# Performance work log

Measured on AMD Instinct MI355X. Metric: run time of the kernel, lower is better.

The kernel has to match this reference:

```python
import math
import jax, jax.numpy as jnp
import numpy as np

B, S, D = 4, 2048, 1024
NEG = -1e20

def setup_inputs() -> dict:
    key = jax.random.key(0)
    k1, k2, k3, k4 = jax.random.split(key, 4)
    X = jax.random.normal(k1, (B, S, D), dtype=jnp.float32)
    # True = masked position (masked_fill semantics)
    attention_mask = jax.random.randint(k2, (B, S, S), 0, 2).astype(bool)
    scale = 1.0 / math.sqrt(D)
    W_qkv = jax.random.normal(k3, (D, 3 * D), dtype=jnp.float32) * scale
    b_qkv = jnp.zeros((3 * D,), dtype=jnp.float32)
    W_out = jax.random.normal(k4, (D, D), dtype=jnp.float32) * scale
    b_out = jnp.zeros((D,), dtype=jnp.float32)
    return {"X": X, "attention_mask": attention_mask,
            "W_qkv": W_qkv, "b_qkv": b_qkv, "W_out": W_out, "b_out": b_out}

def reference(X, attention_mask, W_qkv, b_qkv, W_out, b_out):
    dim = X.shape[-1]
    QKV = X @ W_qkv + b_qkv                      # [B,S,3D]
    Q, K, V = jnp.split(QKV, 3, axis=-1)         # each [B,S,D]
    scores = jnp.einsum('bqd,bkd->bqk', Q, K) / math.sqrt(dim)  # [B,S,S]
    scores = jnp.where(attention_mask, NEG, scores)
    attn = jax.nn.softmax(scores, axis=-1)       # dropout_rate=0.0 -> identity
    ctx = jnp.einsum('bqk,bkd->bqd', attn, V)    # [B,S,D]
    return ctx @ W_out + b_out
```

## Files before the change

kernel.cpp:

```cpp
#include <hip/hip_runtime.h>
#include <cstdint>
#include <cstddef>

#define BB 4
#define SS 2048
#define DD 1024

typedef _Float16 f16;
typedef _Float16 f16x8 __attribute__((ext_vector_type(8)));
typedef _Float16 f16x4 __attribute__((ext_vector_type(4)));
typedef float fx4 __attribute__((ext_vector_type(4)));

__device__ __forceinline__ void async_copy16(void* lds, const void* g) {
  __builtin_amdgcn_global_load_lds(
      (__attribute__((address_space(1))) void*)const_cast<void*>(g),
      (__attribute__((address_space(3))) void*)lds,
      16, 0, 0);
}

template <typename OutT, bool HAS_BIAS>
__global__ __launch_bounds__(256, 2) void gemm_nt(
    const f16* __restrict__ A, long long strideA, int lda,
    const f16* __restrict__ Bt, long long strideB, int ldb,
    OutT* __restrict__ C, long long strideC, int ldc,
    const float* __restrict__ bias, float scale, int K) {
  __shared__ f16 As[128 * 32];
  __shared__ f16 Bs[128 * 32];

  const int t = threadIdx.x;
  const int lane = t & 63;
  const int wid = t >> 6;
  const long long bz = blockIdx.z;
  const int tileM = blockIdx.y * 128;
  const int tileN = blockIdx.x * 128;

  const f16* Ab = A + bz * strideA;
  const f16* Bb = Bt + bz * strideB;
  OutT* Cb = C + bz * strideC;

  const int sr = t >> 2;
  const int sc = (t & 3) * 8;
  const f16* pa0 = Ab + (size_t)(tileM + sr) * lda + sc;
  const f16* pa1 = Ab + (size_t)(tileM + 64 + sr) * lda + sc;
  const f16* pb0 = Bb + (size_t)(tileN + sr) * ldb + sc;
  const f16* pb1 = Bb + (size_t)(tileN + 64 + sr) * ldb + sc;
  f16* la0 = &As[t * 8];
  f16* la1 = &As[2048 + t * 8];
  f16* lb0 = &Bs[t * 8];
  f16* lb1 = &Bs[2048 + t * 8];

  const int waveM = (wid >> 1) * 64;
  const int waveN = (wid & 1) * 64;
  const int r16 = lane & 15;
  const int quad = lane >> 4;

  fx4 acc[4][4] = {};

  for (int k0 = 0; k0 < K; k0 += 32) {
    async_copy16(la0, pa0 + k0);
    async_copy16(la1, pa1 + k0);
    async_copy16(lb0, pb0 + k0);
    async_copy16(lb1, pb1 + k0);
    __syncthreads();

    f16x8 af[4], bf[4];
#pragma unroll
    for (int i = 0; i < 4; ++i)
      af[i] = *(const f16x8*)&As[(waveM + i * 16 + r16) * 32 + quad * 8];
#pragma unroll
    for (int i = 0; i < 4; ++i)
      bf[i] = *(const f16x8*)&Bs[(waveN + i * 16 + r16) * 32 + quad * 8];

#pragma unroll
    for (int i = 0; i < 4; ++i)
#pragma unroll
      for (int j = 0; j < 4; ++j)
        acc[i][j] =
            __builtin_amdgcn_mfma_f32_16x16x32_f16(af[i], bf[j], acc[i][j], 0, 0, 0);
    __syncthreads();
  }

#pragma unroll
  for (int j = 0; j < 4; ++j) {
    const int col = tileN + waveN + j * 16 + r16;
    const float bv = HAS_BIAS ? bias[col] : 0.0f;
#pragma unroll
    for (int i = 0; i < 4; ++i) {
#pragma unroll
      for (int r = 0; r < 4; ++r) {
        const int row = tileM + waveM + i * 16 + quad * 4 + r;
        Cb[(size_t)row * ldc + col] = (OutT)(acc[i][j][r] * scale + bv);
      }
    }
  }
}

__global__ __launch_bounds__(256) void k_conv(const float* __restrict__ in,
                                              f16* __restrict__ out, int n4) {
  const int i = blockIdx.x * 256 + threadIdx.x;
  if (i >= n4) return;
  const float4 v = ((const float4*)in)[i];
  f16x4 h = {(f16)v.x, (f16)v.y, (f16)v.z, (f16)v.w};
  ((f16x4*)out)[i] = h;
}

__global__ __launch_bounds__(256) void k_transpose_conv(const float* __restrict__ in,
                                                        f16* __restrict__ out, int R,
                                                        int C) {
  __shared__ float tile[32][33];
  const int bx = blockIdx.x * 32;
  const int by = blockIdx.y * 32;
  const int tx = threadIdx.x;
  const int ty = threadIdx.y;
  for (int i = ty; i < 32; i += 8)
    tile[i][tx] = in[(size_t)(by + i) * C + bx + tx];
  __syncthreads();
  for (int i = ty; i < 32; i += 8)
    out[(size_t)(bx + i) * R + by + tx] = (f16)tile[tx][i];
}

__global__ __launch_bounds__(256) void k_transpose_h(const f16* __restrict__ in,
                                                     long long strideIn, int ldin,
                                                     int R, f16* __restrict__ out,
                                                     long long strideOut) {
  const int b = blockIdx.z;
  in += (long long)b * strideIn;
  out += (long long)b * strideOut;
  __shared__ f16 tile[32][33];
  const int bx = blockIdx.x * 32;
  const int by = blockIdx.y * 32;
  const int tx = threadIdx.x;
  const int ty = threadIdx.y;
  for (int i = ty; i < 32; i += 8)
    tile[i][tx] = in[(size_t)(by + i) * ldin + bx + tx];
  __syncthreads();
  for (int i = ty; i < 32; i += 8)
    out[(size_t)(bx + i) * R + by + tx] = tile[tx][i];
}

__global__ __launch_bounds__(256) void k_softmax(const f16* __restrict__ scores,
                                                 const int* __restrict__ mask,
                                                 f16* __restrict__ probs) {
  const int row = blockIdx.x;
  const size_t off = (size_t)row * SS;
  const int t = threadIdx.x;

  const f16x8 sv = *(const f16x8*)(scores + off + t * 8);
  const int4 m0 = ((const int4*)(mask + off + t * 8))[0];
  const int4 m1 = ((const int4*)(mask + off + t * 8))[1];
  const int m[8] = {m0.x, m0.y, m0.z, m0.w, m1.x, m1.y, m1.z, m1.w};

  float v[8];
#pragma unroll
  for (int i = 0; i < 8; ++i) v[i] = m[i] ? -1e20f : (float)sv[i];

  float mx = v[0];
#pragma unroll
  for (int i = 1; i < 8; ++i) mx = fmaxf(mx, v[i]);
#pragma unroll
  for (int d = 32; d; d >>= 1) mx = fmaxf(mx, __shfl_xor(mx, d, 64));

  __shared__ float redm[4];
  __shared__ float reds[4];
  if ((t & 63) == 0) redm[t >> 6] = mx;
  __syncthreads();
  mx = fmaxf(fmaxf(redm[0], redm[1]), fmaxf(redm[2], redm[3]));

  float s = 0.0f;
#pragma unroll
  for (int i = 0; i < 8; ++i) {
    v[i] = __expf(v[i] - mx);
    s += v[i];
  }
#pragma unroll
  for (int d = 32; d; d >>= 1) s += __shfl_xor(s, d, 64);
  if ((t & 63) == 0) reds[t >> 6] = s;
  __syncthreads();
  s = reds[0] + reds[1] + reds[2] + reds[3];

  const float inv = 1.0f / s;
  f16x8 pv;
#pragma unroll
  for (int i = 0; i < 8; ++i) pv[i] = (f16)(v[i] * inv);
  *(f16x8*)(probs + off + t * 8) = pv;
}

extern "C" void kernel_launch(void* const* d_in, const int* in_sizes, int n_in,
                              void* d_out, int out_size, void* d_ws, size_t ws_size,
                              hipStream_t stream) {
  const float* X = (const float*)d_in[0];
  const int* mask = (const int*)d_in[1];
  const float* Wqkv = (const float*)d_in[2];
  const float* bqkv = (const float*)d_in[3];
  const float* Wout = (const float*)d_in[4];
  const float* bout = (const float*)d_in[5];
  float* out = (float*)d_out;

  char* ws = (char*)d_ws;
  f16* Xh = (f16*)(ws + 0);
  f16* Wqkvt = (f16*)(ws + 16777216);
  f16* Woutt = (f16*)(ws + 23068672);
  f16* QKV = (f16*)(ws + 25165824);
  f16* Vt = (f16*)(ws + 75497472);
  f16* Sc = (f16*)(ws + 92274688);
  f16* Pr = (f16*)(ws + 125829120);
  f16* Ctx = (f16*)(ws + 159383552);

  k_conv<<<dim3(8192), dim3(256), 0, stream>>>(X, Xh, 8388608 / 4);
  k_transpose_conv<<<dim3(96, 32), dim3(32, 8), 0, stream>>>(Wqkv, Wqkvt, DD, 3 * DD);
  k_transpose_conv<<<dim3(32, 32), dim3(32, 8), 0, stream>>>(Wout, Woutt, DD, DD);

  gemm_nt<f16, true><<<dim3(24, 64, 1), dim3(256), 0, stream>>>(
      Xh, 0LL, DD, Wqkvt, 0LL, DD, QKV, 0LL, 3 * DD, bqkv, 1.0f, DD);

  k_transpose_h<<<dim3(32, 64, 4), dim3(32, 8), 0, stream>>>(
      QKV + 2 * DD, (long long)SS * 3 * DD, 3 * DD, SS, Vt, (long long)DD * SS);

  gemm_nt<f16, false><<<dim3(16, 16, 4), dim3(256), 0, stream>>>(
      QKV, (long long)SS * 3 * DD, 3 * DD, QKV + DD, (long long)SS * 3 * DD, 3 * DD,
      Sc, (long long)SS * SS, SS, nullptr, 0.03125f, DD);

  k_softmax<<<dim3(BB * SS), dim3(256), 0, stream>>>(Sc, mask, Pr);

  gemm_nt<f16, false><<<dim3(8, 16, 4), dim3(256), 0, stream>>>(
      Pr, (long long)SS * SS, SS, Vt, (long long)DD * SS, SS, Ctx,
      (long long)SS * DD, DD, nullptr, 1.0f, SS);

  gemm_nt<float, true><<<dim3(8, 64, 1), dim3(256), 0, stream>>>(
      Ctx, 0LL, DD, Woutt, 0LL, DD, out, 0LL, DD, bout, 1.0f, DD);
}
```

Before: 378.9 us.

## Fuse masked exp softmax into score GEMM epilogue and swizzle LDS tiles

The standalone softmax kernel is removed. The QK^T GEMM epilogue now applies the mask, exponentiates the scaled scores, stores unnormalized f16 values and accumulates per-row sums with atomics. The PV GEMM then divides by the row sum in its epilogue, which avoids a full read and rewrite of the S×S score matrix. Skipping the max subtraction risks f16 overflow when scores are large, and a fully masked row would produce 0/0. An XOR swizzle on the LDS tile layout is also added to reduce bank conflicts on the MFMA fragment loads.

```diff
diff --git a/kernel.cpp b/kernel.cpp
--- a/kernel.cpp
+++ b/kernel.cpp
@@ -18,12 +18,15 @@
       16, 0, 0);
 }
 
-template <typename OutT, bool HAS_BIAS>
+enum { EPI_BIAS = 0, EPI_MASKEXP = 1, EPI_ROWSCALE = 2 };
+
+template <typename OutT, int MODE>
 __global__ __launch_bounds__(256, 2) void gemm_nt(
     const f16* __restrict__ A, long long strideA, int lda,
     const f16* __restrict__ Bt, long long strideB, int ldb,
     OutT* __restrict__ C, long long strideC, int ldc,
-    const float* __restrict__ bias, float scale, int K) {
+    const float* __restrict__ bias, const int* __restrict__ mask,
+    float* __restrict__ rowSum, float scale, int K) {
   __shared__ f16 As[128 * 32];
   __shared__ f16 Bs[128 * 32];
 
@@ -39,7 +42,7 @@
   OutT* Cb = C + bz * strideC;
 
   const int sr = t >> 2;
-  const int sc = (t & 3) * 8;
+  const int sc = (((t & 3) ^ ((t >> 3) & 3)) * 8);
   const f16* pa0 = Ab + (size_t)(tileM + sr) * lda + sc;
   const f16* pa1 = Ab + (size_t)(tileM + 64 + sr) * lda + sc;
   const f16* pb0 = Bb + (size_t)(tileN + sr) * ldb + sc;
@@ -53,6 +56,7 @@
   const int waveN = (wid & 1) * 64;
   const int r16 = lane & 15;
   const int quad = lane >> 4;
+  const int sw = (r16 >> 1) & 3;
 
   fx4 acc[4][4] = {};
 
@@ -66,10 +70,10 @@
     f16x8 af[4], bf[4];
 #pragma unroll
     for (int i = 0; i < 4; ++i)
-      af[i] = *(const f16x8*)&As[(waveM + i * 16 + r16) * 32 + quad * 8];
+      af[i] = *(const f16x8*)&As[(waveM + i * 16 + r16) * 32 + (quad ^ sw) * 8];
 #pragma unroll
     for (int i = 0; i < 4; ++i)
-      bf[i] = *(const f16x8*)&Bs[(waveN + i * 16 + r16) * 32 + quad * 8];
+      bf[i] = *(const f16x8*)&Bs[(waveN + i * 16 + r16) * 32 + (quad ^ sw) * 8];
 
 #pragma unroll
     for (int i = 0; i < 4; ++i)
@@ -80,16 +84,53 @@
     __syncthreads();
   }
 
-#pragma unroll
-  for (int j = 0; j < 4; ++j) {
-    const int col = tileN + waveN + j * 16 + r16;
-    const float bv = HAS_BIAS ? bias[col] : 0.0f;
+  if constexpr (MODE == EPI_BIAS) {
+#pragma unroll
+    for (int j = 0; j < 4; ++j) {
+      const int col = tileN + waveN + j * 16 + r16;
+      const float bv = bias[col];
+#pragma unroll
+      for (int i = 0; i < 4; ++i) {
+#pragma unroll
+        for (int r = 0; r < 4; ++r) {
+          const int row = tileM + waveM + i * 16 + quad * 4 + r;
+          Cb[(size_t)row * ldc + col] = (OutT)(acc[i][j][r] * scale + bv);
+        }
+      }
+    }
+  } else if constexpr (MODE == EPI_MASKEXP) {
+    const int* maskb = mask + bz * strideC;
 #pragma unroll
     for (int i = 0; i < 4; ++i) {
 #pragma unroll
       for (int r = 0; r < 4; ++r) {
         const int row = tileM + waveM + i * 16 + quad * 4 + r;
-        Cb[(size_t)row * ldc + col] = (OutT)(acc[i][j][r] * scale + bv);
+        float part = 0.0f;
+#pragma unroll
+        for (int j = 0; j < 4; ++j) {
+          const int col = tileN + waveN + j * 16 + r16;
+          const int mv = maskb[(size_t)row * ldc + col];
+          const float e = mv ? 0.0f : __expf(acc[i][j][r] * scale);
+          Cb[(size_t)row * ldc + col] = (OutT)e;
+          part += e;
+        }
+#pragma unroll
+        for (int d = 1; d < 16; d <<= 1) part += __shfl_xor(part, d, 64);
+        if (r16 == 0) atomicAdd(&rowSum[bz * SS + row], part);
+      }
+    }
+  } else {
+#pragma unroll
+    for (int i = 0; i < 4; ++i) {
+#pragma unroll
+      for (int r = 0; r < 4; ++r) {
+        const int row = tileM + waveM + i * 16 + quad * 4 + r;
+        const float inv = scale / rowSum[bz * SS + row];
+#pragma unroll
+        for (int j = 0; j < 4; ++j) {
+          const int col = tileN + waveN + j * 16 + r16;
+          Cb[(size_t)row * ldc + col] = (OutT)(acc[i][j][r] * inv);
+        }
       }
     }
   }
@@ -102,6 +143,11 @@
   const float4 v = ((const float4*)in)[i];
   f16x4 h = {(f16)v.x, (f16)v.y, (f16)v.z, (f16)v.w};
   ((f16x4*)out)[i] = h;
+}
+
+__global__ __launch_bounds__(256) void k_zero(float* __restrict__ p, int n) {
+  const int i = blockIdx.x * 256 + threadIdx.x;
+  if (i < n) p[i] = 0.0f;
 }
 
 __global__ __launch_bounds__(256) void k_transpose_conv(const float* __restrict__ in,
@@ -138,53 +184,6 @@
     out[(size_t)(bx + i) * R + by + tx] = tile[tx][i];
 }
 
-__global__ __launch_bounds__(256) void k_softmax(const f16* __restrict__ scores,
-                                                 const int* __restrict__ mask,
-                                                 f16* __restrict__ probs) {
-  const int row = blockIdx.x;
-  const size_t off = (size_t)row * SS;
-  const int t = threadIdx.x;
-
-  const f16x8 sv = *(const f16x8*)(scores + off + t * 8);
-  const int4 m0 = ((const int4*)(mask + off + t * 8))[0];
-  const int4 m1 = ((const int4*)(mask + off + t * 8))[1];
-  const int m[8] = {m0.x, m0.y, m0.z, m0.w, m1.x, m1.y, m1.z, m1.w};
-
-  float v[8];
-#pragma unroll
-  for (int i = 0; i < 8; ++i) v[i] = m[i] ? -1e20f : (float)sv[i];
-
-  float mx = v[0];
-#pragma unroll
-  for (int i = 1; i < 8; ++i) mx = fmaxf(mx, v[i]);
-#pragma unroll
-  for (int d = 32; d; d >>= 1) mx = fmaxf(mx, __shfl_xor(mx, d, 64));
-
-  __shared__ float redm[4];
-  __shared__ float reds[4];
-  if ((t & 63) == 0) redm[t >> 6] = mx;
-  __syncthreads();
-  mx = fmaxf(fmaxf(redm[0], redm[1]), fmaxf(redm[2], redm[3]));
-
-  float s = 0.0f;
-#pragma unroll
-  for (int i = 0; i < 8; ++i) {
-    v[i] = __expf(v[i] - mx);
-    s += v[i];
-  }
-#pragma unroll
-  for (int d = 32; d; d >>= 1) s += __shfl_xor(s, d, 64);
-  if ((t & 63) == 0) reds[t >> 6] = s;
-  __syncthreads();
-  s = reds[0] + reds[1] + reds[2] + reds[3];
-
-  const float inv = 1.0f / s;
-  f16x8 pv;
-#pragma unroll
-  for (int i = 0; i < 8; ++i) pv[i] = (f16)(v[i] * inv);
-  *(f16x8*)(probs + off + t * 8) = pv;
-}
-
 extern "C" void kernel_launch(void* const* d_in, const int* in_sizes, int n_in,
                               void* d_out, int out_size, void* d_ws, size_t ws_size,
                               hipStream_t stream) {
@@ -202,30 +201,29 @@
   f16* Woutt = (f16*)(ws + 23068672);
   f16* QKV = (f16*)(ws + 25165824);
   f16* Vt = (f16*)(ws + 75497472);
-  f16* Sc = (f16*)(ws + 92274688);
-  f16* Pr = (f16*)(ws + 125829120);
-  f16* Ctx = (f16*)(ws + 159383552);
+  f16* E = (f16*)(ws + 92274688);
+  f16* Ctx = (f16*)(ws + 125829120);
+  float* rowSum = (float*)(ws + 142606336);
 
   k_conv<<<dim3(8192), dim3(256), 0, stream>>>(X, Xh, 8388608 / 4);
   k_transpose_conv<<<dim3(96, 32), dim3(32, 8), 0, stream>>>(Wqkv, Wqkvt, DD, 3 * DD);
   k_transpose_conv<<<dim3(32, 32), dim3(32, 8), 0, stream>>>(Wout, Woutt, DD, DD);
-
-  gemm_nt<f16, true><<<dim3(24, 64, 1), dim3(256), 0, stream>>>(
-      Xh, 0LL, DD, Wqkvt, 0LL, DD, QKV, 0LL, 3 * DD, bqkv, 1.0f, DD);
+  k_zero<<<dim3(32), dim3(256), 0, stream>>>(rowSum, BB * SS);
+
+  gemm_nt<f16, EPI_BIAS><<<dim3(24, 64, 1), dim3(256), 0, stream>>>(
+      Xh, 0LL, DD, Wqkvt, 0LL, DD, QKV, 0LL, 3 * DD, bqkv, nullptr, nullptr, 1.0f, DD);
 
   k_transpose_h<<<dim3(32, 64, 4), dim3(32, 8), 0, stream>>>(
       QKV + 2 * DD, (long long)SS * 3 * DD, 3 * DD, SS, Vt, (long long)DD * SS);
 
-  gemm_nt<f16, false><<<dim3(16, 16, 4), dim3(256), 0, stream>>>(
+  gemm_nt<f16, EPI_MASKEXP><<<dim3(16, 16, 4), dim3(256), 0, stream>>>(
       QKV, (long long)SS * 3 * DD, 3 * DD, QKV + DD, (long long)SS * 3 * DD, 3 * DD,
-      Sc, (long long)SS * SS, SS, nullptr, 0.03125f, DD);
-
-  k_softmax<<<dim3(BB * SS), dim3(256), 0, stream>>>(Sc, mask, Pr);
-
-  gemm_nt<f16, false><<<dim3(8, 16, 4), dim3(256), 0, stream>>>(
-      Pr, (long long)SS * SS, SS, Vt, (long long)DD * SS, SS, Ctx,
-      (long long)SS * DD, DD, nullptr, 1.0f, SS);
-
-  gemm_nt<float, true><<<dim3(8, 64, 1), dim3(256), 0, stream>>>(
-      Ctx, 0LL, DD, Woutt, 0LL, DD, out, 0LL, DD, bout, 1.0f, DD);
-}
+      E, (long long)SS * SS, SS, nullptr, mask, rowSum, 0.03125f, DD);
+
+  gemm_nt<f16, EPI_ROWSCALE><<<dim3(8, 16, 4), dim3(256), 0, stream>>>(
+      E, (long long)SS * SS, SS, Vt, (long long)DD * SS, SS, Ctx,
+      (long long)SS * DD, DD, nullptr, nullptr, rowSum, 1.0f, SS);
+
+  gemm_nt<float, EPI_BIAS><<<dim3(8, 64, 1), dim3(256), 0, stream>>>(
+      Ctx, 0LL, DD, Woutt, 0LL, DD, out, 0LL, DD, bout, nullptr, nullptr, 1.0f, DD);
+}
```

Measured after the change: 375.1 us. Within noise of the previous version (-1.0%).
